# Kernel tuning notes

Measured on AMD Instinct MI355X. Metric: run time of the kernel, lower is better.

The kernel has to match this reference:

```python
import jax, jax.numpy as jnp
import numpy as np

WS = 7
NHEAD = 8


def setup_inputs() -> dict:
    key = jax.random.key(0)
    k1, k2, k3 = jax.random.split(key, 3)
    B, H, W, D = 32, 56, 56, 256
    x = jax.random.normal(k1, (B, H, W, D), dtype=jnp.float32)
    in_proj_w = jax.random.normal(k2, (3 * D, D), dtype=jnp.float32) * 0.02
    in_proj_b = jnp.zeros((3 * D,), dtype=jnp.float32)
    out_w = jax.random.normal(k3, (D, D), dtype=jnp.float32) * 0.02
    out_b = jnp.zeros((D,), dtype=jnp.float32)
    return {"x": x, "in_proj_w": in_proj_w, "in_proj_b": in_proj_b,
            "out_w": out_w, "out_b": out_b}


def reference(x, in_proj_w, in_proj_b, out_w, out_b):
    B, Hf, Wf, D = x.shape
    ws = WS
    hd = D // NHEAD
    pad_h = (-Hf) % ws
    pad_w = (-Wf) % ws
    xp = jnp.pad(x, ((0, 0), (0, pad_h), (0, pad_w), (0, 0)))
    Hp, Wp = Hf + pad_h, Wf + pad_w
    nh, nw = Hp // ws, Wp // ws
    # partition into windows: [B*nh*nw, ws*ws, D]
    xw = xp.reshape(B, nh, ws, nw, ws, D).transpose(0, 1, 3, 2, 4, 5)
    xw = xw.reshape(B * nh * nw, ws * ws, D)
    N, L = xw.shape[0], ws * ws
    # qkv projection (torch MHA: x @ in_proj_w.T + in_proj_b)
    qkv = jnp.einsum('nld,ed->nle', xw, in_proj_w) + in_proj_b  # [N, L, 3D]
    q, k, v = jnp.split(qkv, 3, axis=-1)
    q = q.reshape(N, L, NHEAD, hd).transpose(0, 2, 1, 3)
    k = k.reshape(N, L, NHEAD, hd).transpose(0, 2, 1, 3)
    v = v.reshape(N, L, NHEAD, hd).transpose(0, 2, 1, 3)
    scale = 1.0 / np.sqrt(hd).astype(np.float32)
    scores = jnp.einsum('nhqd,nhkd->nhqk', q * scale, k)  # [N, H, L, L]
    attn = jax.nn.softmax(scores, axis=-1)
    o = jnp.einsum('nhqk,nhkd->nhqd', attn, v)
    o = o.transpose(0, 2, 1, 3).reshape(N, L, D)
    o = jnp.einsum('nld,ed->nle', o, out_w) + out_b
    # un-window
    o = o.reshape(B, nh, nw, ws, ws, D).transpose(0, 1, 3, 2, 4, 5)
    o = o.reshape(B, Hp, Wp, D)
    return o[:, :Hf, :Wf, :]
```

## Files before the change

kernel.cpp:

```cpp
#include <hip/hip_runtime.h>


using f16   = _Float16;
using f16x4 = __attribute__((ext_vector_type(4))) _Float16;
using f16x8 = __attribute__((ext_vector_type(8))) _Float16;
using f32x4 = __attribute__((ext_vector_type(4))) float;

#define NTOK   100352
#define DMODEL 256
#define QKVN   768
#define QKV_BYTES 154140672ull
#define WO_HALVES 65536

typedef const __attribute__((address_space(1))) unsigned int* as1_u32p;
typedef __attribute__((address_space(3))) unsigned int* as3_u32p;

__device__ __forceinline__ void gload16(const void* g, void* l) {
    __builtin_amdgcn_global_load_lds((as1_u32p)g, (as3_u32p)l, 16, 0, 0);
}

__device__ __forceinline__ f16x8 zero8() {
    f16x8 z;
#pragma unroll
    for (int i = 0; i < 8; ++i) z[i] = (f16)0;
    return z;
}

#define XV4   6422528
#define WQV4  49152
#define WOV4  16384
__global__ __launch_bounds__(256) void convert_all(
    const float* __restrict__ X, const float* __restrict__ Wq,
    const float* __restrict__ Wo,
    f16* __restrict__ Xh, f16* __restrict__ Wqh, f16* __restrict__ Woh)
{
    const float scale = 0.17677669529663687f;
    const int total = XV4 + WQV4 + WOV4;
    for (int i = blockIdx.x * blockDim.x + threadIdx.x; i < total;
         i += gridDim.x * blockDim.x) {
        float4 f;
        f16x4 h;
        if (i < XV4) {
            f = reinterpret_cast<const float4*>(X)[i];
            h[0]=(f16)f.x; h[1]=(f16)f.y; h[2]=(f16)f.z; h[3]=(f16)f.w;
            reinterpret_cast<f16x4*>(Xh)[i] = h;
        } else if (i < XV4 + WQV4) {
            int idx = i - XV4;
            int row = idx >> 6;
            float sc = (row < 256) ? scale : 1.0f;
            f = reinterpret_cast<const float4*>(Wq)[idx];
            h[0]=(f16)(f.x*sc); h[1]=(f16)(f.y*sc); h[2]=(f16)(f.z*sc); h[3]=(f16)(f.w*sc);
            reinterpret_cast<f16x4*>(Wqh)[idx] = h;
        } else if (Woh) {
            int idx = i - XV4 - WQV4;
            f = reinterpret_cast<const float4*>(Wo)[idx];
            h[0]=(f16)f.x; h[1]=(f16)f.y; h[2]=(f16)f.z; h[3]=(f16)f.w;
            reinterpret_cast<f16x4*>(Woh)[idx] = h;
        }
    }
}

__global__ __launch_bounds__(256) void qkv_gemm(
    const f16* __restrict__ Xh,
    const f16* __restrict__ Wh,
    const float* __restrict__ bias,
    f16* __restrict__ QKV)
{
    __shared__ f16 As[128 * 64];
    __shared__ f16 Bs[128 * 64];
    const int tid  = threadIdx.x;
    const int lane = tid & 63;
    const int wave = tid >> 6;
    int wg = blockIdx.x;
    const int cpx = (NTOK / 128) * (QKVN / 128) / 8;
    wg = (wg & 7) * cpx + (wg >> 3);
    const int m0 = (wg / (QKVN / 128)) * 128;
    const int n0 = (wg % (QKVN / 128)) * 128;
    const int wm = (wave >> 1) * 64;
    const int wn = (wave & 1) * 64;
    const int g  = lane >> 4;
    const int lr = lane & 15;

    f32x4 acc[4][4] = {};

    for (int k0 = 0; k0 < 256; k0 += 64) {
#pragma unroll
        for (int j = 0; j < 4; ++j) {
            int s   = tid + j * 256;
            int row = s >> 3, sl = s & 7;
            int ss  = sl ^ (row & 7);
            gload16(Xh + (size_t)(m0 + row) * 256 + k0 + ss * 8, &As[s * 8]);
            gload16(Wh + (size_t)(n0 + row) * 256 + k0 + ss * 8, &Bs[s * 8]);
        }
        __syncthreads();
#pragma unroll
        for (int ks = 0; ks < 2; ++ks) {
            f16x8 a[4], b[4];
#pragma unroll
            for (int i = 0; i < 4; ++i) {
                int row = wm + i * 16 + lr;
                int c   = ((ks << 2) + g) ^ (row & 7);
                a[i] = *reinterpret_cast<const f16x8*>(&As[row * 64 + c * 8]);
            }
#pragma unroll
            for (int i = 0; i < 4; ++i) {
                int row = wn + i * 16 + lr;
                int c   = ((ks << 2) + g) ^ (row & 7);
                b[i] = *reinterpret_cast<const f16x8*>(&Bs[row * 64 + c * 8]);
            }
#pragma unroll
            for (int mi = 0; mi < 4; ++mi)
#pragma unroll
                for (int ni = 0; ni < 4; ++ni)
                    acc[mi][ni] = __builtin_amdgcn_mfma_f32_16x16x32_f16(a[mi], b[ni], acc[mi][ni], 0, 0, 0);
        }
        __syncthreads();
    }
    const float scale = 0.17677669529663687f;
#pragma unroll
    for (int ni = 0; ni < 4; ++ni) {
        int n = n0 + wn + ni * 16 + lr;
        float bv = bias[n];
        if (n < 256) bv *= scale;
#pragma unroll
        for (int mi = 0; mi < 4; ++mi)
#pragma unroll
            for (int r = 0; r < 4; ++r) {
                int m = m0 + wm + mi * 16 + g * 4 + r;
                QKV[(size_t)m * QKVN + n] = (f16)(acc[mi][ni][r] + bv);
            }
    }
}

__global__ __launch_bounds__(256) void win_attn(f16* __restrict__ QKV)
{
    __shared__ f16 Vt[4][32][68];
    __shared__ f16 P[4][64][68];
    const int tid  = threadIdx.x;
    const int lane = tid & 63;
    const int w    = tid >> 6;
    const int u    = blockIdx.x * 4 + w;
    const int win = u >> 3, h = u & 7;
    const int b = win >> 6, wh = (win >> 3) & 7, ww = win & 7;
    const int base = (b * 56 + wh * 7) * 56 + ww * 7;
    const int g = lane >> 4, lr = lane & 15;

    auto tok = [&](int row) { int rr = row / 7; return base + rr * 56 + (row - rr * 7); };

    f16x8 qf[4], kf[4];
#pragma unroll
    for (int i = 0; i < 4; ++i) {
        int row = i * 16 + lr;
        if (row < 49) {
            size_t off = (size_t)tok(row) * QKVN + h * 32 + g * 8;
            qf[i] = *reinterpret_cast<const f16x8*>(QKV + off);
            kf[i] = *reinterpret_cast<const f16x8*>(QKV + off + 256);
        } else { qf[i] = zero8(); kf[i] = zero8(); }
    }
    {
        int kk = lane;
        if (kk < 49) {
            size_t off = (size_t)tok(kk) * QKVN + 512 + h * 32;
            f16x8 vv[4];
#pragma unroll
            for (int j = 0; j < 4; ++j)
                vv[j] = *reinterpret_cast<const f16x8*>(QKV + off + j * 8);
#pragma unroll
            for (int j = 0; j < 4; ++j)
#pragma unroll
                for (int d = 0; d < 8; ++d) Vt[w][j * 8 + d][kk] = vv[j][d];
        } else {
#pragma unroll
            for (int d = 0; d < 32; ++d) Vt[w][d][kk] = (f16)0;
        }
    }
    f32x4 s[4][4] = {};
#pragma unroll
    for (int ki = 0; ki < 4; ++ki)
#pragma unroll
        for (int qi = 0; qi < 4; ++qi)
            s[ki][qi] = __builtin_amdgcn_mfma_f32_16x16x32_f16(kf[ki], qf[qi], s[ki][qi], 0, 0, 0);

#pragma unroll
    for (int qi = 0; qi < 4; ++qi) {
        float e[4][4];
        float sum = 0.f;
#pragma unroll
        for (int ki = 0; ki < 4; ++ki)
#pragma unroll
            for (int r = 0; r < 4; ++r)
                e[ki][r] = __expf(s[ki][qi][r]);
#pragma unroll
        for (int ki = 0; ki < 3; ++ki)
#pragma unroll
            for (int r = 0; r < 4; ++r)
                sum += e[ki][r];
        sum += (g == 0) ? e[3][0] : 0.f;
        sum += __shfl_xor(sum, 16, 64);
        sum += __shfl_xor(sum, 32, 64);
        float is = 1.f / sum;
#pragma unroll
        for (int ki = 0; ki < 4; ++ki) {
            f16x4 pw;
            pw[0] = (f16)(e[ki][0] * is);
            pw[1] = (f16)(e[ki][1] * is);
            pw[2] = (f16)(e[ki][2] * is);
            pw[3] = (f16)(e[ki][3] * is);
            *reinterpret_cast<f16x4*>(&P[w][qi * 16 + lr][ki * 16 + g * 4]) = pw;
        }
    }
    __syncthreads();

    f32x4 o[4][2] = {};
#pragma unroll
    for (int ks = 0; ks < 2; ++ks) {
        f16x8 pa[4], vb[2];
#pragma unroll
        for (int mi = 0; mi < 4; ++mi)
            pa[mi] = *reinterpret_cast<const f16x8*>(&P[w][mi * 16 + lr][ks * 32 + g * 8]);
#pragma unroll
        for (int ni = 0; ni < 2; ++ni)
            vb[ni] = *reinterpret_cast<const f16x8*>(&Vt[w][ni * 16 + lr][ks * 32 + g * 8]);
#pragma unroll
        for (int mi = 0; mi < 4; ++mi)
#pragma unroll
            for (int ni = 0; ni < 2; ++ni)
                o[mi][ni] = __builtin_amdgcn_mfma_f32_16x16x32_f16(pa[mi], vb[ni], o[mi][ni], 0, 0, 0);
    }
#pragma unroll
    for (int mi = 0; mi < 4; ++mi)
#pragma unroll
        for (int r = 0; r < 4; ++r) {
            int row = mi * 16 + g * 4 + r;
            if (row < 49) {
                size_t off = (size_t)tok(row) * QKVN + h * 32;
#pragma unroll
                for (int ni = 0; ni < 2; ++ni)
                    QKV[off + ni * 16 + lr] = (f16)o[mi][ni][r];
            }
        }
}

__global__ __launch_bounds__(256) void out_gemm_f16(
    const f16* __restrict__ O,
    const f16* __restrict__ Wh,
    const float* __restrict__ bias,
    float* __restrict__ OUT)
{
    __shared__ f16 As[128 * 64];
    __shared__ f16 Bs[128 * 64];
    const int tid  = threadIdx.x;
    const int lane = tid & 63;
    const int wave = tid >> 6;
    int wg = blockIdx.x;
    const int cpx = (NTOK / 128) * (DMODEL / 128) / 8;
    wg = (wg & 7) * cpx + (wg >> 3);
    const int m0 = (wg / (DMODEL / 128)) * 128;
    const int n0 = (wg % (DMODEL / 128)) * 128;
    const int wm = (wave >> 1) * 64;
    const int wn = (wave & 1) * 64;
    const int g  = lane >> 4;
    const int lr = lane & 15;

    f32x4 acc[4][4] = {};

    for (int k0 = 0; k0 < 256; k0 += 64) {
#pragma unroll
        for (int j = 0; j < 4; ++j) {
            int s   = tid + j * 256;
            int row = s >> 3, sl = s & 7;
            int ss  = sl ^ (row & 7);
            gload16(O + (size_t)(m0 + row) * QKVN + k0 + ss * 8, &As[s * 8]);
            gload16(Wh + (size_t)(n0 + row) * 256 + k0 + ss * 8, &Bs[s * 8]);
        }
        __syncthreads();
#pragma unroll
        for (int ks = 0; ks < 2; ++ks) {
            f16x8 a[4], b[4];
#pragma unroll
            for (int i = 0; i < 4; ++i) {
                int row = wm + i * 16 + lr;
                int c   = ((ks << 2) + g) ^ (row & 7);
                a[i] = *reinterpret_cast<const f16x8*>(&As[row * 64 + c * 8]);
            }
#pragma unroll
            for (int i = 0; i < 4; ++i) {
                int row = wn + i * 16 + lr;
                int c   = ((ks << 2) + g) ^ (row & 7);
                b[i] = *reinterpret_cast<const f16x8*>(&Bs[row * 64 + c * 8]);
            }
#pragma unroll
            for (int mi = 0; mi < 4; ++mi)
#pragma unroll
                for (int ni = 0; ni < 4; ++ni)
                    acc[mi][ni] = __builtin_amdgcn_mfma_f32_16x16x32_f16(a[mi], b[ni], acc[mi][ni], 0, 0, 0);
        }
        __syncthreads();
    }
#pragma unroll
    for (int ni = 0; ni < 4; ++ni) {
        int n = n0 + wn + ni * 16 + lr;
        float bv = bias[n];
#pragma unroll
        for (int mi = 0; mi < 4; ++mi)
#pragma unroll
            for (int r = 0; r < 4; ++r) {
                int m = m0 + wm + mi * 16 + g * 4 + r;
                OUT[(size_t)m * 256 + n] = acc[mi][ni][r] + bv;
            }
    }
}

__global__ __launch_bounds__(256) void out_gemm_cvt(
    const f16* __restrict__ O,
    const float* __restrict__ W,
    const float* __restrict__ bias,
    float* __restrict__ OUT)
{
    __shared__ f16 As[128 * 64];
    __shared__ f16 Bs[128][72];
    const int tid  = threadIdx.x;
    const int lane = tid & 63;
    const int wave = tid >> 6;
    int wg = blockIdx.x;
    const int cpx = (NTOK / 128) * (DMODEL / 128) / 8;
    wg = (wg & 7) * cpx + (wg >> 3);
    const int m0 = (wg / (DMODEL / 128)) * 128;
    const int n0 = (wg % (DMODEL / 128)) * 128;
    const int wm = (wave >> 1) * 64;
    const int wn = (wave & 1) * 64;
    const int g  = lane >> 4;
    const int lr = lane & 15;

    f32x4 acc[4][4] = {};

    for (int k0 = 0; k0 < 256; k0 += 64) {
#pragma unroll
        for (int j = 0; j < 4; ++j) {
            int s   = tid + j * 256;
            int row = s >> 3, sl = s & 7;
            int ss  = sl ^ (row & 7);
            gload16(O + (size_t)(m0 + row) * QKVN + k0 + ss * 8, &As[s * 8]);
        }
#pragma unroll
        for (int j = 0; j < 8; ++j) {
            int v = tid + j * 256;
            int row = v >> 4, cv = v & 15;
            float4 f = *reinterpret_cast<const float4*>(W + (size_t)(n0 + row) * 256 + k0 + cv * 4);
            f16x4 h; h[0]=(f16)f.x; h[1]=(f16)f.y; h[2]=(f16)f.z; h[3]=(f16)f.w;
            *reinterpret_cast<f16x4*>(&Bs[row][cv * 4]) = h;
        }
        __syncthreads();
#pragma unroll
        for (int ks = 0; ks < 2; ++ks) {
            f16x8 a[4], b[4];
#pragma unroll
            for (int i = 0; i < 4; ++i) {
                int row = wm + i * 16 + lr;
                int c   = ((ks << 2) + g) ^ (row & 7);
                a[i] = *reinterpret_cast<const f16x8*>(&As[row * 64 + c * 8]);
            }
#pragma unroll
            for (int i = 0; i < 4; ++i)
                b[i] = *reinterpret_cast<const f16x8*>(&Bs[wn + i * 16 + lr][ks * 32 + g * 8]);
#pragma unroll
            for (int mi = 0; mi < 4; ++mi)
#pragma unroll
                for (int ni = 0; ni < 4; ++ni)
                    acc[mi][ni] = __builtin_amdgcn_mfma_f32_16x16x32_f16(a[mi], b[ni], acc[mi][ni], 0, 0, 0);
        }
        __syncthreads();
    }
#pragma unroll
    for (int ni = 0; ni < 4; ++ni) {
        int n = n0 + wn + ni * 16 + lr;
        float bv = bias[n];
#pragma unroll
        for (int mi = 0; mi < 4; ++mi)
#pragma unroll
            for (int r = 0; r < 4; ++r) {
                int m = m0 + wm + mi * 16 + g * 4 + r;
                OUT[(size_t)m * 256 + n] = acc[mi][ni][r] + bv;
            }
    }
}

extern "C" void kernel_launch(void* const* d_in, const int* in_sizes, int n_in,
                              void* d_out, int out_size, void* d_ws, size_t ws_size,
                              hipStream_t stream) {
    const float* x     = (const float*)d_in[0];
    const float* in_w  = (const float*)d_in[1];
    const float* in_b  = (const float*)d_in[2];
    const float* out_w = (const float*)d_in[3];
    const float* out_b = (const float*)d_in[4];
    float* out = (float*)d_out;
    f16* qkv = (f16*)d_ws;

    f16* xh  = (f16*)d_out;
    f16* wqh = xh + (size_t)NTOK * 256;
    const bool tailok = ws_size >= QKV_BYTES + (size_t)WO_HALVES * 2;
    f16* woh = tailok ? (f16*)((char*)d_ws + QKV_BYTES) : nullptr;

    convert_all<<<2048, 256, 0, stream>>>(x, in_w, out_w, xh, wqh, woh);

    qkv_gemm<<<(NTOK / 128) * (QKVN / 128), 256, 0, stream>>>(xh, wqh, in_b, qkv);

    win_attn<<<4096, 256, 0, stream>>>(qkv);

    if (tailok)
        out_gemm_f16<<<(NTOK / 128) * (DMODEL / 128), 256, 0, stream>>>(qkv, woh, out_b, out);
    else
        out_gemm_cvt<<<(NTOK / 128) * (DMODEL / 128), 256, 0, stream>>>(qkv, out_w, out_b, out);
}
```

Before: 149.6 us.

## Fuse QKV projection into window attention kernel per window-head

Merges the QKV GEMM with window attention. Each block stages one window's 49 tokens of X in LDS and computes the Q, K and V projections for four heads, with weight fragments read straight from global memory. The attention output then goes to a compact 256-wide buffer that the output GEMM reads. This removes the round trip of the full QKV tensor through HBM. The cost is that the input projection is now done with small 49-row tiles, so each block reloads its weight slices (served by L2), MFMA utilisation is lower, and LDS use per block rises.

```diff
diff --git a/kernel.cpp b/kernel.cpp
--- a/kernel.cpp
+++ b/kernel.cpp
@@ -9,7 +9,7 @@
 #define NTOK   100352
 #define DMODEL 256
 #define QKVN   768
-#define QKV_BYTES 154140672ull
+#define OH_BYTES 51380224ull
 #define WO_HALVES 65536
 
 typedef const __attribute__((address_space(1))) unsigned int* as1_u32p;
@@ -60,120 +60,117 @@
     }
 }
 
-__global__ __launch_bounds__(256) void qkv_gemm(
+__global__ __launch_bounds__(256) void qkv_attn(
     const f16* __restrict__ Xh,
-    const f16* __restrict__ Wh,
+    const f16* __restrict__ Wqh,
     const float* __restrict__ bias,
-    f16* __restrict__ QKV)
+    f16* __restrict__ Oh)
 {
-    __shared__ f16 As[128 * 64];
-    __shared__ f16 Bs[128 * 64];
-    const int tid  = threadIdx.x;
-    const int lane = tid & 63;
-    const int wave = tid >> 6;
-    int wg = blockIdx.x;
-    const int cpx = (NTOK / 128) * (QKVN / 128) / 8;
-    wg = (wg & 7) * cpx + (wg >> 3);
-    const int m0 = (wg / (QKVN / 128)) * 128;
-    const int n0 = (wg % (QKVN / 128)) * 128;
-    const int wm = (wave >> 1) * 64;
-    const int wn = (wave & 1) * 64;
-    const int g  = lane >> 4;
-    const int lr = lane & 15;
-
-    f32x4 acc[4][4] = {};
-
-    for (int k0 = 0; k0 < 256; k0 += 64) {
-#pragma unroll
-        for (int j = 0; j < 4; ++j) {
-            int s   = tid + j * 256;
-            int row = s >> 3, sl = s & 7;
-            int ss  = sl ^ (row & 7);
-            gload16(Xh + (size_t)(m0 + row) * 256 + k0 + ss * 8, &As[s * 8]);
-            gload16(Wh + (size_t)(n0 + row) * 256 + k0 + ss * 8, &Bs[s * 8]);
-        }
-        __syncthreads();
-#pragma unroll
-        for (int ks = 0; ks < 2; ++ks) {
-            f16x8 a[4], b[4];
-#pragma unroll
-            for (int i = 0; i < 4; ++i) {
-                int row = wm + i * 16 + lr;
-                int c   = ((ks << 2) + g) ^ (row & 7);
-                a[i] = *reinterpret_cast<const f16x8*>(&As[row * 64 + c * 8]);
-            }
-#pragma unroll
-            for (int i = 0; i < 4; ++i) {
-                int row = wn + i * 16 + lr;
-                int c   = ((ks << 2) + g) ^ (row & 7);
-                b[i] = *reinterpret_cast<const f16x8*>(&Bs[row * 64 + c * 8]);
-            }
-#pragma unroll
-            for (int mi = 0; mi < 4; ++mi)
-#pragma unroll
-                for (int ni = 0; ni < 4; ++ni)
-                    acc[mi][ni] = __builtin_amdgcn_mfma_f32_16x16x32_f16(a[mi], b[ni], acc[mi][ni], 0, 0, 0);
-        }
-        __syncthreads();
-    }
-    const float scale = 0.17677669529663687f;
-#pragma unroll
-    for (int ni = 0; ni < 4; ++ni) {
-        int n = n0 + wn + ni * 16 + lr;
-        float bv = bias[n];
-        if (n < 256) bv *= scale;
-#pragma unroll
-        for (int mi = 0; mi < 4; ++mi)
-#pragma unroll
-            for (int r = 0; r < 4; ++r) {
-                int m = m0 + wm + mi * 16 + g * 4 + r;
-                QKV[(size_t)m * QKVN + n] = (f16)(acc[mi][ni][r] + bv);
-            }
-    }
-}
-
-__global__ __launch_bounds__(256) void win_attn(f16* __restrict__ QKV)
-{
+    __shared__ f16 Xw[49 * 256];
+    __shared__ f16 P[4][64][68];
     __shared__ f16 Vt[4][32][68];
-    __shared__ f16 P[4][64][68];
     const int tid  = threadIdx.x;
     const int lane = tid & 63;
     const int w    = tid >> 6;
-    const int u    = blockIdx.x * 4 + w;
-    const int win = u >> 3, h = u & 7;
+    const int bx   = blockIdx.x;
+    const int win  = bx >> 1;
+    const int h    = ((bx & 1) << 2) + w;
     const int b = win >> 6, wh = (win >> 3) & 7, ww = win & 7;
     const int base = (b * 56 + wh * 7) * 56 + ww * 7;
     const int g = lane >> 4, lr = lane & 15;
+    const float scale = 0.17677669529663687f;
 
     auto tok = [&](int row) { int rr = row / 7; return base + rr * 56 + (row - rr * 7); };
 
-    f16x8 qf[4], kf[4];
-#pragma unroll
-    for (int i = 0; i < 4; ++i) {
-        int row = i * 16 + lr;
-        if (row < 49) {
-            size_t off = (size_t)tok(row) * QKVN + h * 32 + g * 8;
-            qf[i] = *reinterpret_cast<const f16x8*>(QKV + off);
-            kf[i] = *reinterpret_cast<const f16x8*>(QKV + off + 256);
-        } else { qf[i] = zero8(); kf[i] = zero8(); }
-    }
+#pragma unroll
+    for (int i = 0; i < 7; ++i) {
+        int s = tid + i * 256;
+        if (s < 1568) {
+            int row = s >> 5, sl = s & 31;
+            int ss  = sl ^ (row & 31);
+            gload16(Xh + (size_t)tok(row) * 256 + ss * 8, &Xw[s * 8]);
+        }
+    }
+    __syncthreads();
+
+    auto chunk = [&](int sec, f32x4 (&acc)[4][2]) {
+        const f16* Ws = Wqh + (size_t)((sec << 8) + (h << 5)) * 256;
+#pragma unroll
+        for (int kstep = 0; kstep < 8; ++kstep) {
+            f16x8 a[4], bf[2];
+#pragma unroll
+            for (int mi = 0; mi < 4; ++mi) {
+                int row = mi * 16 + lr;
+                if (row < 49) {
+                    int sl = ((kstep << 2) + g) ^ (row & 31);
+                    a[mi] = *reinterpret_cast<const f16x8*>(&Xw[row * 256 + sl * 8]);
+                } else a[mi] = zero8();
+            }
+#pragma unroll
+            for (int nb = 0; nb < 2; ++nb)
+                bf[nb] = *reinterpret_cast<const f16x8*>(
+                    Ws + (size_t)(nb * 16 + lr) * 256 + (kstep << 5) + g * 8);
+#pragma unroll
+            for (int mi = 0; mi < 4; ++mi)
+#pragma unroll
+                for (int nb = 0; nb < 2; ++nb)
+                    acc[mi][nb] = __builtin_amdgcn_mfma_f32_16x16x32_f16(a[mi], bf[nb], acc[mi][nb], 0, 0, 0);
+        }
+    };
+
+    f16x8 kf[4], qf[4];
     {
-        int kk = lane;
-        if (kk < 49) {
-            size_t off = (size_t)tok(kk) * QKVN + 512 + h * 32;
-            f16x8 vv[4];
-#pragma unroll
-            for (int j = 0; j < 4; ++j)
-                vv[j] = *reinterpret_cast<const f16x8*>(QKV + off + j * 8);
-#pragma unroll
-            for (int j = 0; j < 4; ++j)
-#pragma unroll
-                for (int d = 0; d < 8; ++d) Vt[w][j * 8 + d][kk] = vv[j][d];
-        } else {
-#pragma unroll
-            for (int d = 0; d < 32; ++d) Vt[w][d][kk] = (f16)0;
-        }
-    }
+        f32x4 acc[4][2] = {};
+        chunk(1, acc);
+        float bv[2] = { bias[256 + h * 32 + lr], bias[256 + h * 32 + 16 + lr] };
+#pragma unroll
+        for (int nb = 0; nb < 2; ++nb)
+#pragma unroll
+            for (int mi = 0; mi < 4; ++mi)
+#pragma unroll
+                for (int r = 0; r < 4; ++r) {
+                    int row = mi * 16 + g * 4 + r;
+                    P[w][row][nb * 16 + lr] =
+                        (row < 49) ? (f16)(acc[mi][nb][r] + bv[nb]) : (f16)0;
+                }
+#pragma unroll
+        for (int i = 0; i < 4; ++i)
+            kf[i] = *reinterpret_cast<const f16x8*>(&P[w][i * 16 + lr][g * 8]);
+    }
+    {
+        f32x4 acc[4][2] = {};
+        chunk(0, acc);
+        float bv[2] = { bias[h * 32 + lr] * scale, bias[h * 32 + 16 + lr] * scale };
+#pragma unroll
+        for (int nb = 0; nb < 2; ++nb)
+#pragma unroll
+            for (int mi = 0; mi < 4; ++mi)
+#pragma unroll
+                for (int r = 0; r < 4; ++r) {
+                    int row = mi * 16 + g * 4 + r;
+                    P[w][row][nb * 16 + lr] =
+                        (row < 49) ? (f16)(acc[mi][nb][r] + bv[nb]) : (f16)0;
+                }
+#pragma unroll
+        for (int i = 0; i < 4; ++i)
+            qf[i] = *reinterpret_cast<const f16x8*>(&P[w][i * 16 + lr][g * 8]);
+    }
+    {
+        f32x4 acc[4][2] = {};
+        chunk(2, acc);
+        float bv[2] = { bias[512 + h * 32 + lr], bias[512 + h * 32 + 16 + lr] };
+#pragma unroll
+        for (int nb = 0; nb < 2; ++nb)
+#pragma unroll
+            for (int mi = 0; mi < 4; ++mi)
+#pragma unroll
+                for (int r = 0; r < 4; ++r) {
+                    int row = mi * 16 + g * 4 + r;
+                    Vt[w][nb * 16 + lr][row] =
+                        (row < 49) ? (f16)(acc[mi][nb][r] + bv[nb]) : (f16)0;
+                }
+    }
+
     f32x4 s[4][4] = {};
 #pragma unroll
     for (int ki = 0; ki < 4; ++ki)
@@ -209,7 +206,6 @@
             *reinterpret_cast<f16x4*>(&P[w][qi * 16 + lr][ki * 16 + g * 4]) = pw;
         }
     }
-    __syncthreads();
 
     f32x4 o[4][2] = {};
 #pragma unroll
@@ -233,10 +229,10 @@
         for (int r = 0; r < 4; ++r) {
             int row = mi * 16 + g * 4 + r;
             if (row < 49) {
-                size_t off = (size_t)tok(row) * QKVN + h * 32;
+                size_t off = (size_t)tok(row) * 256 + h * 32;
 #pragma unroll
                 for (int ni = 0; ni < 2; ++ni)
-                    QKV[off + ni * 16 + lr] = (f16)o[mi][ni][r];
+                    Oh[off + ni * 16 + lr] = (f16)o[mi][ni][r];
             }
         }
 }
@@ -270,7 +266,7 @@
             int s   = tid + j * 256;
             int row = s >> 3, sl = s & 7;
             int ss  = sl ^ (row & 7);
-            gload16(O + (size_t)(m0 + row) * QKVN + k0 + ss * 8, &As[s * 8]);
+            gload16(O + (size_t)(m0 + row) * 256 + k0 + ss * 8, &As[s * 8]);
             gload16(Wh + (size_t)(n0 + row) * 256 + k0 + ss * 8, &Bs[s * 8]);
         }
         __syncthreads();
@@ -340,7 +336,7 @@
             int s   = tid + j * 256;
             int row = s >> 3, sl = s & 7;
             int ss  = sl ^ (row & 7);
-            gload16(O + (size_t)(m0 + row) * QKVN + k0 + ss * 8, &As[s * 8]);
+            gload16(O + (size_t)(m0 + row) * 256 + k0 + ss * 8, &As[s * 8]);
         }
 #pragma unroll
         for (int j = 0; j < 8; ++j) {
@@ -394,21 +390,20 @@
     const float* out_w = (const float*)d_in[3];
     const float* out_b = (const float*)d_in[4];
     float* out = (float*)d_out;
-    f16* qkv = (f16*)d_ws;
+
+    f16* oh = (f16*)d_ws;
+    const bool tailok = ws_size >= OH_BYTES + (size_t)WO_HALVES * 2;
+    f16* woh = tailok ? (f16*)((char*)d_ws + OH_BYTES) : nullptr;
 
     f16* xh  = (f16*)d_out;
     f16* wqh = xh + (size_t)NTOK * 256;
-    const bool tailok = ws_size >= QKV_BYTES + (size_t)WO_HALVES * 2;
-    f16* woh = tailok ? (f16*)((char*)d_ws + QKV_BYTES) : nullptr;
 
     convert_all<<<2048, 256, 0, stream>>>(x, in_w, out_w, xh, wqh, woh);
 
-    qkv_gemm<<<(NTOK / 128) * (QKVN / 128), 256, 0, stream>>>(xh, wqh, in_b, qkv);
-
-    win_attn<<<4096, 256, 0, stream>>>(qkv);
+    qkv_attn<<<4096, 256, 0, stream>>>(xh, wqh, in_b, oh);
 
     if (tailok)
-        out_gemm_f16<<<(NTOK / 128) * (DMODEL / 128), 256, 0, stream>>>(qkv, woh, out_b, out);
+        out_gemm_f16<<<(NTOK / 128) * (DMODEL / 128), 256, 0, stream>>>(oh, woh, out_b, out);
     else
-        out_gemm_cvt<<<(NTOK / 128) * (DMODEL / 128), 256, 0, stream>>>(qkv, out_w, out_b, out);
-}
+        out_gemm_cvt<<<(NTOK / 128) * (DMODEL / 128), 256, 0, stream>>>(oh, out_w, out_b, out);
+}
```

Result: slower. 171.3 us (+14.5%).
